# Optimization experiments

Hardware: AMD Instinct MI355X
Metric: run time of the kernel (lower is better)

## Reference

```python
import jax, jax.numpy as jnp
import numpy as np

EMBED_DIM = 1024
NUM_HEADS = 16
HEAD_DIM = EMBED_DIM // NUM_HEADS
FF_DIM = 4096
EPS = 1e-5


def layer_norm(x, gamma, beta):
    mu = jnp.mean(x, axis=-1, keepdims=True)
    var = jnp.var(x, axis=-1, keepdims=True)
    return (x - mu) * jax.lax.rsqrt(var + EPS) * gamma + beta


def setup_inputs() -> dict:
    key = jax.random.key(0)
    ks = jax.random.split(key, 10)
    B, S = 2, 2048
    sd = 1.0 / np.sqrt(EMBED_DIM)
    sf = 1.0 / np.sqrt(FF_DIM)
    return {
        "x": jax.random.normal(ks[0], (B, S, EMBED_DIM), jnp.float32),
        # grouped QKV: 3*num_heads groups, each embed_dim -> head_dim
        "Wqkv": jax.random.normal(ks[1], (3 * NUM_HEADS, EMBED_DIM, HEAD_DIM), jnp.float32) * sd,
        "bqkv": jnp.zeros((3 * NUM_HEADS, HEAD_DIM), jnp.float32),
        "Wo": jax.random.normal(ks[2], (EMBED_DIM, EMBED_DIM), jnp.float32) * sd,
        "bo": jnp.zeros((EMBED_DIM,), jnp.float32),
        "W1": jax.random.normal(ks[3], (EMBED_DIM, FF_DIM), jnp.float32) * sd,
        "b1": jnp.zeros((FF_DIM,), jnp.float32),
        "W2": jax.random.normal(ks[4], (FF_DIM, EMBED_DIM), jnp.float32) * sf,
        "b2": jnp.zeros((EMBED_DIM,), jnp.float32),
        "ln1_g": jnp.ones((EMBED_DIM,), jnp.float32),
        "ln1_b": jnp.zeros((EMBED_DIM,), jnp.float32),
        "ln2_g": jnp.ones((EMBED_DIM,), jnp.float32),
        "ln2_b": jnp.zeros((EMBED_DIM,), jnp.float32),
    }


def reference(x, Wqkv, bqkv, Wo, bo, W1, b1, W2, b2, ln1_g, ln1_b, ln2_g, ln2_b):
    B, S, D = x.shape
    normed = layer_norm(x, ln1_g, ln1_b)
    # grouped QKV projection: group g gets its own (D, head_dim) weight
    qkv = jnp.einsum('bsd,gdh->bgsh', normed, Wqkv) + bqkv[None, :, None, :]
    qkv = qkv.reshape(B, 3, NUM_HEADS, S, HEAD_DIM)
    q, k, v = qkv[:, 0], qkv[:, 1], qkv[:, 2]  # each [B, H, S, hd]
    attn = jnp.einsum('bhqd,bhkd->bhqk', q, k) / np.sqrt(HEAD_DIM)
    attn = jax.nn.softmax(attn, axis=-1)
    out = jnp.einsum('bhqk,bhkd->bhqd', attn, v)
    out = out.transpose(0, 2, 1, 3).reshape(B, S, D)
    out = out @ Wo + bo
    x = x + out
    normed2 = layer_norm(x, ln2_g, ln2_b)
    ff = jax.nn.relu(normed2 @ W1 + b1) @ W2 + b2
    return x + ff
```

## Files before the change

kernel.cpp:

```cpp
#include <hip/hip_runtime.h>
#include <stdint.h>

#define SEQ    2048
#define NB     2
#define NHEADS 16
#define HDIM   64
#define EMBED  1024
#define NROWS  (NB*SEQ)
#define QKVSZ  ((size_t)NB*NHEADS*SEQ*HDIM)

typedef __attribute__((ext_vector_type(8))) short short8;
typedef __attribute__((ext_vector_type(4))) float float4v;
typedef __attribute__((ext_vector_type(16))) float float16v;
typedef __attribute__((ext_vector_type(2))) unsigned int uint2v;
typedef __attribute__((ext_vector_type(4))) unsigned int uint4v;

__device__ __forceinline__ float b2f(unsigned short h) {
    unsigned int u = ((unsigned int)h) << 16;
    union { unsigned int u; float f; } c; c.u = u; return c.f;
}
__device__ __forceinline__ unsigned short f2b(float f) {
    union { float f; unsigned int u; } c; c.f = f;
    unsigned int u = c.u;
    u += 0x7FFFu + ((u >> 16) & 1u);
    return (unsigned short)(u >> 16);
}
__device__ __forceinline__ unsigned int fbits(float f) {
    union { float f; unsigned int u; } c; c.f = f; return c.u;
}
__device__ __forceinline__ unsigned int cvtpk_bf16(float lo, float hi) {
    unsigned int r;
    asm("v_cvt_pk_bf16_f32 %0, %1, %2" : "=v"(r) : "v"(lo), "v"(hi));
    return r;
}

__device__ __forceinline__ void gload_lds16(const void* g, void* l) {
    __builtin_amdgcn_global_load_lds(
        (const __attribute__((address_space(1))) unsigned int*)g,
        (__attribute__((address_space(3))) unsigned int*)l, 16, 0, 0);
}

__device__ __forceinline__ int probe_f32(const void* probe) {
    return ((const unsigned short*)probe)[0] == 0;
}
__device__ __forceinline__ float lde(const void* base, size_t off, int f32) {
    return f32 ? ((const float*)base)[off] : b2f(((const unsigned short*)base)[off]);
}
__device__ __forceinline__ void ste(void* base, size_t off, float v, int f32) {
    if (f32) ((float*)base)[off] = v;
    else     ((unsigned short*)base)[off] = f2b(v);
}

__global__ __launch_bounds__(256) void ln_kernel(
    const void* __restrict__ x,
    const void* __restrict__ g,
    const void* __restrict__ b,
    unsigned short* __restrict__ out,
    const void* __restrict__ probe)
{
    int f32 = probe_f32(probe);
    int row = blockIdx.x;
    int t = threadIdx.x;
    float v0, v1, v2, v3;
    if (f32) {
        float4 rv = ((const float4*)x)[(size_t)row * (EMBED / 4) + t];
        v0 = rv.x; v1 = rv.y; v2 = rv.z; v3 = rv.w;
    } else {
        ushort4 rv = ((const ushort4*)((const unsigned short*)x + (size_t)row * EMBED))[t];
        v0 = b2f(rv.x); v1 = b2f(rv.y); v2 = b2f(rv.z); v3 = b2f(rv.w);
    }
    float s  = v0 + v1 + v2 + v3;
    float sq = v0*v0 + v1*v1 + v2*v2 + v3*v3;
    #pragma unroll
    for (int off = 32; off > 0; off >>= 1) {
        s  += __shfl_xor(s,  off);
        sq += __shfl_xor(sq, off);
    }
    __shared__ float red[8];
    int lane = t & 63, wv = t >> 6;
    if (lane == 0) { red[wv] = s; red[wv + 4] = sq; }
    __syncthreads();
    s  = red[0] + red[1] + red[2] + red[3];
    sq = red[4] + red[5] + red[6] + red[7];
    float mu  = s * (1.0f / EMBED);
    float var = sq * (1.0f / EMBED) - mu * mu;
    float rs  = rsqrtf(var + 1e-5f);
    float g0 = lde(g, t*4+0, f32), g1 = lde(g, t*4+1, f32);
    float g2 = lde(g, t*4+2, f32), g3 = lde(g, t*4+3, f32);
    float b0 = lde(b, t*4+0, f32), b1 = lde(b, t*4+1, f32);
    float b2 = lde(b, t*4+2, f32), b3 = lde(b, t*4+3, f32);
    ushort4 ov;
    ov.x = f2b((v0 - mu) * rs * g0 + b0);
    ov.y = f2b((v1 - mu) * rs * g1 + b1);
    ov.z = f2b((v2 - mu) * rs * g2 + b2);
    ov.w = f2b((v3 - mu) * rs * g3 + b3);
    ((ushort4*)(out + (size_t)row * EMBED))[t] = ov;
}

template<int QKV>
__global__ __launch_bounds__(256) void transpose_kernel(
    const void* __restrict__ in,
    unsigned short* __restrict__ out, int K, int N,
    const void* __restrict__ probe)
{
    __shared__ unsigned short t[64 * 68];
    int f32 = probe_f32(probe);
    int tid = threadIdx.x;
    int n0 = blockIdx.x * 64, k0 = blockIdx.y * 64;
    #pragma unroll
    for (int i = 0; i < 4; i++) {
        int id = tid + i * 256;
        int kr = id >> 4, nc = (id & 15) * 4;
        size_t srcoff;
        if (QKV) srcoff = ((size_t)(n0 >> 6) << 16) + (size_t)(k0 + kr) * 64 + nc;
        else     srcoff = (size_t)(k0 + kr) * N + n0 + nc;
        ushort4 val;
        if (f32) {
            float4 rv = *(const float4*)((const float*)in + srcoff);
            val.x = f2b(rv.x); val.y = f2b(rv.y); val.z = f2b(rv.z); val.w = f2b(rv.w);
        } else {
            val = *(const ushort4*)((const unsigned short*)in + srcoff);
        }
        *(ushort4*)&t[kr * 68 + nc] = val;
    }
    __syncthreads();
    #pragma unroll
    for (int i = 0; i < 4; i++) {
        int id = tid + i * 256;
        int nr = id >> 4, kc = (id & 15) * 4;
        ushort4 o;
        o.x = t[(kc + 0) * 68 + nr];
        o.y = t[(kc + 1) * 68 + nr];
        o.z = t[(kc + 2) * 68 + nr];
        o.w = t[(kc + 3) * 68 + nr];
        *(ushort4*)(out + (size_t)(n0 + nr) * K + k0 + kc) = o;
    }
}

template<int DO_RELU, int HAS_BIAS, int OUTMODE>
__global__ __launch_bounds__(512) void gemm256_kernel(
    const unsigned short* __restrict__ A,
    const unsigned short* __restrict__ Bt,
    const void* __restrict__ bias,
    void* __restrict__ out,
    int M, int N, int Kloc, int ldA, int ldB,
    const void* __restrict__ probe)
{
    __shared__ unsigned short Als[2][256 * 64];
    __shared__ unsigned short Bls[2][256 * 64];
    int f32 = probe_f32(probe);
    int tid = threadIdx.x;
    int lane = tid & 63, wv = tid >> 6;
    int lq = lane >> 4, lr = lane & 15;
    int wr = wv >> 2, wc = wv & 3;
    int m0 = blockIdx.y * 256, n0 = blockIdx.x * 256;
    int k0 = blockIdx.z * Kloc;

    int srow = tid >> 3;
    int sch  = (tid & 7) ^ (srow & 7);
    const unsigned short* ga = A  + (size_t)(m0 + srow) * ldA + k0 + sch * 8;
    const unsigned short* gb = Bt + (size_t)(n0 + srow) * ldB + k0 + sch * 8;
    int ldst = tid * 8;
    int rx = lr & 7;

    float4v acc[8][4];
    #pragma unroll
    for (int i = 0; i < 8; i++)
        #pragma unroll
        for (int j = 0; j < 4; j++)
            { acc[i][j][0] = 0.f; acc[i][j][1] = 0.f; acc[i][j][2] = 0.f; acc[i][j][3] = 0.f; }

    int nkt = Kloc >> 6;
    #pragma unroll
    for (int u = 0; u < 4; u++)
        gload_lds16(ga + (size_t)u * 64 * ldA, &Als[0][u * 4096 + ldst]);
    #pragma unroll
    for (int u = 0; u < 4; u++)
        gload_lds16(gb + (size_t)u * 64 * ldB, &Bls[0][u * 4096 + ldst]);

    for (int kt = 0; kt < nkt; kt++) {
        int cur = kt & 1, nxt = cur ^ 1;
        if (kt + 1 < nkt) {
            int ko = (kt + 1) * 64;
            #pragma unroll
            for (int u = 0; u < 4; u++)
                gload_lds16(ga + (size_t)u * 64 * ldA + ko, &Als[nxt][u * 4096 + ldst]);
            asm volatile("s_waitcnt vmcnt(4)" ::: "memory");
        } else {
            asm volatile("s_waitcnt vmcnt(0)" ::: "memory");
        }
        __builtin_amdgcn_s_barrier();
        asm volatile("" ::: "memory");
        {
            short8 af[8], bf[4];
            #pragma unroll
            for (int mt = 0; mt < 8; mt++)
                af[mt] = *(const short8*)(
                    &Als[cur][(wr * 128 + mt * 16 + lr) * 64 + ((lq ^ rx) * 8)]);
            #pragma unroll
            for (int nt = 0; nt < 4; nt++)
                bf[nt] = *(const short8*)(
                    &Bls[cur][(wc * 64 + nt * 16 + lr) * 64 + ((lq ^ rx) * 8)]);
            __builtin_amdgcn_s_setprio(1);
            #pragma unroll
            for (int mt = 0; mt < 8; mt++)
                #pragma unroll
                for (int nt = 0; nt < 4; nt++)
                    acc[mt][nt] = __builtin_amdgcn_mfma_f32_16x16x32_bf16(af[mt], bf[nt], acc[mt][nt], 0, 0, 0);
            __builtin_amdgcn_s_setprio(0);
        }
        if (kt + 1 < nkt) {
            int ko = (kt + 1) * 64;
            #pragma unroll
            for (int u = 0; u < 4; u++)
                gload_lds16(gb + (size_t)u * 64 * ldB + ko, &Bls[nxt][u * 4096 + ldst]);
        }
        {
            short8 af[8], bf[4];
            #pragma unroll
            for (int mt = 0; mt < 8; mt++)
                af[mt] = *(const short8*)(
                    &Als[cur][(wr * 128 + mt * 16 + lr) * 64 + (((4 + lq) ^ rx) * 8)]);
            #pragma unroll
            for (int nt = 0; nt < 4; nt++)
                bf[nt] = *(const short8*)(
                    &Bls[cur][(wc * 64 + nt * 16 + lr) * 64 + (((4 + lq) ^ rx) * 8)]);
            __builtin_amdgcn_s_setprio(1);
            #pragma unroll
            for (int mt = 0; mt < 8; mt++)
                #pragma unroll
                for (int nt = 0; nt < 4; nt++)
                    acc[mt][nt] = __builtin_amdgcn_mfma_f32_16x16x32_bf16(af[mt], bf[nt], acc[mt][nt], 0, 0, 0);
            __builtin_amdgcn_s_setprio(0);
        }
        asm volatile("s_waitcnt lgkmcnt(0)" ::: "memory");
        __builtin_amdgcn_s_barrier();
    }

    if (OUTMODE == 3) {
        float* po = (float*)out + (size_t)blockIdx.z * M * N;
        #pragma unroll
        for (int mt = 0; mt < 8; mt++)
            #pragma unroll
            for (int nt = 0; nt < 4; nt++)
                #pragma unroll
                for (int rg = 0; rg < 4; rg++) {
                    int rr = m0 + wr * 128 + mt * 16 + lq * 4 + rg;
                    int cc = n0 + wc * 64 + nt * 16 + lr;
                    po[(size_t)rr * N + cc] = acc[mt][nt][rg];
                }
    } else if (OUTMODE == 2) {
        #pragma unroll
        for (int mt = 0; mt < 8; mt++) {
            int rrb = m0 + wr * 128 + mt * 16 + lq * 4;
            int bb = rrb >> 11, ss = rrb & 2047;
            #pragma unroll
            for (int nt = 0; nt < 4; nt++) {
                int cc = n0 + wc * 64 + nt * 16 + lr;
                int gg = cc >> 6, hd = cc & 63;
                int ty = gg >> 4, hh = gg & 15;
                float vv[4];
                #pragma unroll
                for (int rg = 0; rg < 4; rg++) {
                    float v = acc[mt][nt][rg];
                    if (HAS_BIAS) v += lde(bias, (size_t)cc, f32);
                    vv[rg] = v;
                }
                if (ty < 2) {
                    unsigned short* p = (unsigned short*)out + (size_t)ty * QKVSZ +
                        (((size_t)(bb * NHEADS + hh) * SEQ + ss) * HDIM) + hd;
                    #pragma unroll
                    for (int rg = 0; rg < 4; rg++) p[(size_t)rg * HDIM] = f2b(vv[rg]);
                } else {
                    ushort4 pk;
                    pk.x = f2b(vv[0]); pk.y = f2b(vv[1]);
                    pk.z = f2b(vv[2]); pk.w = f2b(vv[3]);
                    *(ushort4*)((unsigned short*)out + 2 * QKVSZ +
                        ((size_t)(bb * NHEADS + hh) * HDIM + hd) * SEQ + ss) = pk;
                }
            }
        }
    } else {
        #pragma unroll
        for (int mt = 0; mt < 8; mt++)
            #pragma unroll
            for (int nt = 0; nt < 4; nt++)
                #pragma unroll
                for (int rg = 0; rg < 4; rg++) {
                    int rr = m0 + wr * 128 + mt * 16 + lq * 4 + rg;
                    int cc = n0 + wc * 64 + nt * 16 + lr;
                    float v = acc[mt][nt][rg];
                    if (HAS_BIAS) v += lde(bias, (size_t)cc, f32);
                    if (DO_RELU) v = v > 0.f ? v : 0.f;
                    ((unsigned short*)out)[(size_t)rr * N + cc] = f2b(v);
                }
    }
}

template<int DO_RELU, int HAS_BIAS, int OUTMODE>
__global__ __launch_bounds__(512) void gemm256p8_kernel(
    const unsigned short* __restrict__ A,
    const unsigned short* __restrict__ Bt,
    const void* __restrict__ bias,
    void* __restrict__ out,
    int M, int N, int Kloc, int ldA, int ldB,
    const void* __restrict__ probe)
{
    __shared__ unsigned short Als[2][2][128 * 64];
    __shared__ unsigned short Bls[2][2][128 * 64];
    int f32 = probe_f32(probe);
    int tid = threadIdx.x;
    int lane = tid & 63, wv = tid >> 6;
    int lq = lane >> 4, lr = lane & 15;
    int wr = wv >> 2, wc = wv & 3;
    int m0 = blockIdx.y * 256, n0 = blockIdx.x * 256;
    int k0 = blockIdx.z * Kloc;

    int srow = tid >> 3;
    int sch  = (tid & 7) ^ (srow & 7);
    const unsigned short* ga = A  + (size_t)(m0 + srow) * ldA + k0 + sch * 8;
    const unsigned short* gb = Bt + (size_t)(n0 + srow) * ldB + k0 + sch * 8;
    int ldst = tid * 8;
    int rx = lr & 7;

    auto stA = [&](int d, int h, int ko) {
        gload_lds16(ga + (size_t)(h * 128) * ldA + ko, &Als[d][h][ldst]);
        gload_lds16(ga + (size_t)(h * 128 + 64) * ldA + ko, &Als[d][h][4096 + ldst]);
    };
    auto stB = [&](int d, int h, int ko) {
        gload_lds16(gb + (size_t)(h * 128) * ldB + ko, &Bls[d][h][ldst]);
        gload_lds16(gb + (size_t)(h * 128 + 64) * ldB + ko, &Bls[d][h][4096 + ldst]);
    };
    auto rdA = [&](int d, int qm, short8 (&af)[4][2]) {
        #pragma unroll
        for (int mt = 0; mt < 4; mt++)
            #pragma unroll
            for (int c = 0; c < 2; c++)
                af[mt][c] = *(const short8*)(&Als[d][qm][
                    (wr * 64 + mt * 16 + lr) * 64 + (((c * 4 + lq) ^ rx) * 8)]);
    };
    auto rdB = [&](int d, int qn, short8 (&bf)[2][2]) {
        #pragma unroll
        for (int nt = 0; nt < 2; nt++)
            #pragma unroll
            for (int c = 0; c < 2; c++)
                bf[nt][c] = *(const short8*)(&Bls[d][qn][
                    (wc * 32 + nt * 16 + lr) * 64 + (((c * 4 + lq) ^ rx) * 8)]);
    };
    auto MM = [&](short8 (&af)[4][2], short8 (&bf)[2][2], float4v (&aq)[4][2]) {
        __builtin_amdgcn_s_setprio(1);
        #pragma unroll
        for (int c = 0; c < 2; c++)
            #pragma unroll
            for (int mt = 0; mt < 4; mt++)
                #pragma unroll
                for (int nt = 0; nt < 2; nt++)
                    aq[mt][nt] = __builtin_amdgcn_mfma_f32_16x16x32_bf16(
                        af[mt][c], bf[nt][c], aq[mt][nt], 0, 0, 0);
        __builtin_amdgcn_s_setprio(0);
    };
    #define VMC(n)  asm volatile("s_waitcnt vmcnt(" #n ")" ::: "memory")
    #define BARF()  do { __builtin_amdgcn_s_barrier(); \
                         asm volatile("" ::: "memory"); } while (0)

    float4v acc00[4][2], acc01[4][2], acc11[4][2], acc10[4][2];
    #pragma unroll
    for (int i = 0; i < 4; i++)
        #pragma unroll
        for (int j = 0; j < 2; j++) {
            acc00[i][j] = float4v{0.f, 0.f, 0.f, 0.f};
            acc01[i][j] = float4v{0.f, 0.f, 0.f, 0.f};
            acc11[i][j] = float4v{0.f, 0.f, 0.f, 0.f};
            acc10[i][j] = float4v{0.f, 0.f, 0.f, 0.f};
        }
    short8 af0[4][2], af1[4][2], bf0[2][2], bf1[2][2];

    int nkt = Kloc >> 6;
    int npair = nkt >> 1;

    stA(0, 0, 0); stB(0, 0, 0); stB(0, 1, 0); stA(0, 1, 0);
    VMC(4); BARF();
    rdA(0, 0, af0); rdB(0, 0, bf0);

    for (int p = 0; p < npair - 1; p++) {
        int koB  = (2 * p + 1) * 64;
        int koA2 = (2 * p + 2) * 64;
        MM(af0, bf0, acc00); stA(1, 0, koB); VMC(4); BARF(); rdB(0, 1, bf1);
        MM(af0, bf1, acc01); stB(1, 0, koB); VMC(4); BARF(); rdA(0, 1, af1);
        MM(af1, bf1, acc11); stB(1, 1, koB);         BARF(); rdB(0, 0, bf0);
        MM(af1, bf0, acc10); stA(1, 1, koB); VMC(4); BARF(); rdA(1, 0, af0); rdB(1, 0, bf1);
        MM(af0, bf1, acc00); stA(0, 0, koA2); VMC(4); BARF(); rdB(1, 1, bf0);
        MM(af0, bf0, acc01); stB(0, 0, koA2); VMC(4); BARF(); rdA(1, 1, af1);
        MM(af1, bf0, acc11); stB(0, 1, koA2);         BARF(); rdB(1, 0, bf1);
        MM(af1, bf1, acc10); stA(0, 1, koA2); VMC(4); BARF(); rdA(0, 0, af0); rdB(0, 0, bf0);
    }
    {
        int koB = (nkt - 1) * 64;
        MM(af0, bf0, acc00); stA(1, 0, koB); VMC(4); BARF(); rdB(0, 1, bf1);
        MM(af0, bf1, acc01); stB(1, 0, koB); VMC(4); BARF(); rdA(0, 1, af1);
        MM(af1, bf1, acc11); stB(1, 1, koB);         BARF(); rdB(0, 0, bf0);
        MM(af1, bf0, acc10); stA(1, 1, koB); VMC(4); BARF(); rdA(1, 0, af0); rdB(1, 0, bf1);
        MM(af0, bf1, acc00);                  VMC(2); BARF(); rdB(1, 1, bf0);
        MM(af0, bf0, acc01);                  VMC(0); BARF(); rdA(1, 1, af1);
        MM(af1, bf0, acc11);                          BARF(); rdB(1, 0, bf1);
        MM(af1, bf1, acc10);
    }
    #undef VMC
    #undef BARF

    auto storeQ = [&](int qr, int qc, float4v (&aq)[4][2]) {
        if (OUTMODE == 3) {
            float* po = (float*)out + (size_t)blockIdx.z * M * N;
            #pragma unroll
            for (int mt = 0; mt < 4; mt++)
                #pragma unroll
                for (int nt = 0; nt < 2; nt++)
                    #pragma unroll
                    for (int rg = 0; rg < 4; rg++) {
                        int rr = m0 + qr * 128 + wr * 64 + mt * 16 + lq * 4 + rg;
                        int cc = n0 + qc * 128 + wc * 32 + nt * 16 + lr;
                        po[(size_t)rr * N + cc] = aq[mt][nt][rg];
                    }
        } else {
            #pragma unroll
            for (int mt = 0; mt < 4; mt++)
                #pragma unroll
                for (int nt = 0; nt < 2; nt++)
                    #pragma unroll
                    for (int rg = 0; rg < 4; rg++) {
                        int rr = m0 + qr * 128 + wr * 64 + mt * 16 + lq * 4 + rg;
                        int cc = n0 + qc * 128 + wc * 32 + nt * 16 + lr;
                        float v = aq[mt][nt][rg];
                        if (HAS_BIAS) v += lde(bias, (size_t)cc, f32);
                        if (DO_RELU) v = v > 0.f ? v : 0.f;
                        ((unsigned short*)out)[(size_t)rr * N + cc] = f2b(v);
                    }
        }
    };
    storeQ(0, 0, acc00); storeQ(0, 1, acc01);
    storeQ(1, 1, acc11); storeQ(1, 0, acc10);
}

__global__ __launch_bounds__(256) void ff2_combine_kernel(
    const float* __restrict__ part,
    const void* __restrict__ b2,
    void* __restrict__ xout,
    const void* __restrict__ probe)
{
    int f32 = probe_f32(probe);
    int row = blockIdx.x;
    int t = threadIdx.x;
    const size_t MN = (size_t)NROWS * EMBED;
    size_t base = (size_t)row * EMBED + t * 4;
    float4 p0 = *(const float4*)(part + base);
    float4 p1 = *(const float4*)(part + MN + base);
    float4 p2 = *(const float4*)(part + 2 * MN + base);
    float4 p3 = *(const float4*)(part + 3 * MN + base);
    float s0 = (p0.x + p1.x) + (p2.x + p3.x);
    float s1 = (p0.y + p1.y) + (p2.y + p3.y);
    float s2 = (p0.z + p1.z) + (p2.z + p3.z);
    float s3 = (p0.w + p1.w) + (p2.w + p3.w);
    int c = t * 4;
    s0 += lde(b2, c + 0, f32) + lde(xout, base + 0, f32);
    s1 += lde(b2, c + 1, f32) + lde(xout, base + 1, f32);
    s2 += lde(b2, c + 2, f32) + lde(xout, base + 2, f32);
    s3 += lde(b2, c + 3, f32) + lde(xout, base + 3, f32);
    ste(xout, base + 0, s0, f32);
    ste(xout, base + 1, s1, f32);
    ste(xout, base + 2, s2, f32);
    ste(xout, base + 3, s3, f32);
}

template<int DO_RELU, int HAS_BIAS, int HAS_RES, int OUTMODE>
__global__ __launch_bounds__(256) void gemm64_kernel(
    const unsigned short* __restrict__ A,
    const unsigned short* __restrict__ Bt,
    const void* __restrict__ bias,
    const void* __restrict__ res,
    void* __restrict__ out,
    int M, int N, int K, int ldA, int ldB,
    const void* __restrict__ probe)
{
    __shared__ unsigned short Als[2][64 * 32];
    __shared__ unsigned short Bls[2][64 * 32];
    int f32 = probe_f32(probe);
    int tid = threadIdx.x;
    int lane = tid & 63, wv = tid >> 6;
    int lq = lane >> 4, lr = lane & 15;
    int moff = (wv >> 1) * 32, noff = (wv & 1) * 32;
    int m0 = blockIdx.y * 64, n0 = blockIdx.x * 64;

    int rA = tid >> 2, jA = tid & 3;
    int jjA = jA ^ ((rA >> 1) & 3);
    const unsigned short* ga = A  + (size_t)(m0 + rA) * ldA + jjA * 8;
    const unsigned short* gb = Bt + (size_t)(n0 + rA) * ldB + jjA * 8;

    int fch = (lq ^ ((lr >> 1) & 3)) * 8;

    float4v acc[2][2];
    #pragma unroll
    for (int i = 0; i < 2; i++)
        #pragma unroll
        for (int j = 0; j < 2; j++)
            { acc[i][j][0] = 0.f; acc[i][j][1] = 0.f; acc[i][j][2] = 0.f; acc[i][j][3] = 0.f; }

    gload_lds16(ga, &Als[0][(size_t)tid * 8]);
    gload_lds16(gb, &Bls[0][(size_t)tid * 8]);

    int nkt = K >> 5;
    for (int kt = 0; kt < nkt; kt++) {
        int cur = kt & 1, nxt = cur ^ 1;
        __syncthreads();
        if (kt + 1 < nkt) {
            int ko = (kt + 1) * 32;
            gload_lds16(ga + ko, &Als[nxt][(size_t)tid * 8]);
            gload_lds16(gb + ko, &Bls[nxt][(size_t)tid * 8]);
        }
        short8 af[2], bfr[2];
        #pragma unroll
        for (int mt = 0; mt < 2; mt++)
            af[mt] = *(const short8*)(&Als[cur][(moff + mt * 16 + lr) * 32 + fch]);
        #pragma unroll
        for (int nt = 0; nt < 2; nt++)
            bfr[nt] = *(const short8*)(&Bls[cur][(noff + nt * 16 + lr) * 32 + fch]);
        #pragma unroll
        for (int mt = 0; mt < 2; mt++)
            #pragma unroll
            for (int nt = 0; nt < 2; nt++)
                acc[mt][nt] = __builtin_amdgcn_mfma_f32_16x16x32_bf16(af[mt], bfr[nt], acc[mt][nt], 0, 0, 0);
    }

    #pragma unroll
    for (int mt = 0; mt < 2; mt++) {
        #pragma unroll
        for (int nt = 0; nt < 2; nt++) {
            #pragma unroll
            for (int rg = 0; rg < 4; rg++) {
                int rr = m0 + moff + mt * 16 + lq * 4 + rg;
                int cc = n0 + noff + nt * 16 + lr;
                float v = acc[mt][nt][rg];
                if (HAS_BIAS) v += lde(bias, (size_t)cc, f32);
                if (DO_RELU) v = v > 0.f ? v : 0.f;
                if (HAS_RES) v += lde(res, (size_t)rr * N + cc, f32);
                if (OUTMODE == 1) ste(out, (size_t)rr * N + cc, v, f32);
                else ((unsigned short*)out)[(size_t)rr * N + cc] = f2b(v);
            }
        }
    }
}

__global__ __launch_bounds__(512) void attn_kernel(
    const unsigned short* __restrict__ qb,
    const unsigned short* __restrict__ kb,
    const unsigned short* __restrict__ vtb,
    unsigned short* __restrict__ outb)
{
    __shared__ unsigned short Kls[2][2][64 * 64];
    __shared__ unsigned short Vls[2][2][64 * 64];
    int tid = threadIdx.x;
    int lane = tid & 63, wv = tid >> 6;
    int l31 = lane & 31, hh = lane >> 5;
    int qg = wv & 3, half = wv >> 2;
    int bh = blockIdx.y;
    int b = bh >> 4, head = bh & 15;
    const unsigned short* q  = qb  + (size_t)bh * SEQ * HDIM;
    const unsigned short* k  = kb  + (size_t)bh * SEQ * HDIM;
    const unsigned short* vt = vtb + (size_t)bh * HDIM * SEQ;
    int q0w = blockIdx.x * 128 + qg * 32;

    const float C2 = 0.18033688011112042f;

    short8 qf[4];
    #pragma unroll
    for (int c = 0; c < 4; c++) {
        short8 raw = *(const short8*)(q + (size_t)(q0w + l31) * HDIM + c * 16 + hh * 8);
        #pragma unroll
        for (int j = 0; j < 8; j++)
            qf[c][j] = (short)f2b(b2f((unsigned short)raw[j]) * C2);
    }

    int ts = tid & 255;
    int rS = ts >> 3;
    int jjS = (ts & 7) ^ (rS & 7);
    const int NTH = SEQ / 128;
    int tbase = half * NTH;
    const unsigned short* gk0 = k + (size_t)rS * HDIM + jjS * 8;
    const unsigned short* gk1 = k + (size_t)(rS + 32) * HDIM + jjS * 8;
    const unsigned short* gv0 = vt + (size_t)rS * SEQ + jjS * 8;
    const unsigned short* gv1 = vt + (size_t)(rS + 32) * SEQ + jjS * 8;

    auto stage = [&](int bf, int tl) {
        int k0n = (tbase + tl) * 64;
        gload_lds16(gk0 + (size_t)k0n * HDIM, &Kls[half][bf][(size_t)ts * 8]);
        gload_lds16(gk1 + (size_t)k0n * HDIM, &Kls[half][bf][(size_t)(ts + 256) * 8]);
        gload_lds16(gv0 + k0n, &Vls[half][bf][(size_t)ts * 8]);
        gload_lds16(gv1 + k0n, &Vls[half][bf][(size_t)(ts + 256) * 8]);
    };

    float l_part = 0.f;
    float16v o0, o1;
    #pragma unroll
    for (int i = 0; i < 16; i++) { o0[i] = 0.f; o1[i] = 0.f; }

    stage(0, 0);

    for (int t = 0; t < NTH; t++) {
        int cur = t & 1;
        __builtin_amdgcn_s_barrier();
        asm volatile("" ::: "memory");
        if (t + 1 < NTH) {
            stage(cur ^ 1, t + 1);
            asm volatile("s_waitcnt vmcnt(4)" ::: "memory");
        } else {
            asm volatile("s_waitcnt vmcnt(0)" ::: "memory");
        }
        __builtin_amdgcn_s_barrier();
        asm volatile("" ::: "memory");

        float16v st0, st1;
        #pragma unroll
        for (int i = 0; i < 16; i++) { st0[i] = 0.f; st1[i] = 0.f; }
        {
            int r0 = l31, r1 = 32 + l31;
            int rxk = l31 & 7;
            __builtin_amdgcn_s_setprio(1);
            #pragma unroll
            for (int c = 0; c < 4; c++) {
                short8 kf0 = *(const short8*)(
                    &Kls[half][cur][r0 * 64 + (((2 * c + hh) ^ rxk) * 8)]);
                st0 = __builtin_amdgcn_mfma_f32_32x32x16_bf16(kf0, qf[c], st0, 0, 0, 0);
                short8 kf1 = *(const short8*)(
                    &Kls[half][cur][r1 * 64 + (((2 * c + hh) ^ rxk) * 8)]);
                st1 = __builtin_amdgcn_mfma_f32_32x32x16_bf16(kf1, qf[c], st1, 0, 0, 0);
            }
            __builtin_amdgcn_s_setprio(0);
        }

        int rv0 = l31, rv1 = 32 + l31;
        int rxv = l31 & 7;
        #pragma unroll
        for (int kb2 = 0; kb2 < 2; kb2++) {
            float p[16];
            #pragma unroll
            for (int rg = 0; rg < 16; rg++) {
                float sv = kb2 ? st1[rg] : st0[rg];
                p[rg] = __builtin_amdgcn_exp2f(sv);
                l_part += p[rg];
            }
            #pragma unroll
            for (int s = 0; s < 2; s++) {
                unsigned int a1 = cvtpk_bf16(p[8*s+0], p[8*s+1]);
                unsigned int a2 = cvtpk_bf16(p[8*s+2], p[8*s+3]);
                unsigned int b1 = cvtpk_bf16(p[8*s+4], p[8*s+5]);
                unsigned int b2 = cvtpk_bf16(p[8*s+6], p[8*s+7]);
                uint2v r1 = __builtin_amdgcn_permlane32_swap(a1, b1, false, false);
                uint2v r2 = __builtin_amdgcn_permlane32_swap(a2, b2, false, false);
                union { uint4v u; short8 s8; } pun;
                pun.u.x = r1.x; pun.u.y = r2.x; pun.u.z = r1.y; pun.u.w = r2.y;
                short8 pf = pun.s8;
                int g = kb2 * 2 + s;
                short8 vf0 = *(const short8*)(
                    &Vls[half][cur][rv0 * 64 + (((2 * g + hh) ^ rxv) * 8)]);
                short8 vf1 = *(const short8*)(
                    &Vls[half][cur][rv1 * 64 + (((2 * g + hh) ^ rxv) * 8)]);
                __builtin_amdgcn_s_setprio(1);
                o0 = __builtin_amdgcn_mfma_f32_32x32x16_bf16(pf, vf0, o0, 0, 0, 0);
                o1 = __builtin_amdgcn_mfma_f32_32x32x16_bf16(pf, vf1, o1, 0, 0, 0);
                __builtin_amdgcn_s_setprio(0);
            }
        }
    }

    l_part += __shfl_xor(l_part, 32);

    __syncthreads();
    float* obuf = (float*)&Kls[0][0][0];
    float* lbuf = (float*)&Vls[0][0][0];
    if (half == 1) {
        float* od = obuf + (size_t)qg * 2048 + lane * 4;
        #pragma unroll
        for (int ib = 0; ib < 4; ib++) {
            float4 v4;
            v4.x = o0[ib*4+0]; v4.y = o0[ib*4+1]; v4.z = o0[ib*4+2]; v4.w = o0[ib*4+3];
            *(float4*)(od + ib * 256) = v4;
        }
        #pragma unroll
        for (int ib = 0; ib < 4; ib++) {
            float4 v4;
            v4.x = o1[ib*4+0]; v4.y = o1[ib*4+1]; v4.z = o1[ib*4+2]; v4.w = o1[ib*4+3];
            *(float4*)(od + (ib + 4) * 256) = v4;
        }
        if (hh == 0) lbuf[qg * 32 + l31] = l_part;
    }
    __syncthreads();
    if (half == 0) {
        float* od = obuf + (size_t)qg * 2048 + lane * 4;
        #pragma unroll
        for (int ib = 0; ib < 4; ib++) {
            float4 v4 = *(const float4*)(od + ib * 256);
            o0[ib*4+0] += v4.x; o0[ib*4+1] += v4.y; o0[ib*4+2] += v4.z; o0[ib*4+3] += v4.w;
        }
        #pragma unroll
        for (int ib = 0; ib < 4; ib++) {
            float4 v4 = *(const float4*)(od + (ib + 4) * 256);
            o1[ib*4+0] += v4.x; o1[ib*4+1] += v4.y; o1[ib*4+2] += v4.z; o1[ib*4+3] += v4.w;
        }
        float linv_me = 1.f / (l_part + lbuf[qg * 32 + l31]);
        #pragma unroll
        for (int rg = 0; rg < 16; rg++) {
            int qrow = (rg & 3) + 8 * (rg >> 2) + 4 * hh;
            float linv = __shfl(linv_me, qrow);
            size_t rowbase = ((size_t)(b * SEQ + q0w + qrow)) * EMBED + head * HDIM;
            outb[rowbase + l31]      = f2b(o0[rg] * linv);
            outb[rowbase + 32 + l31] = f2b(o1[rg] * linv);
        }
    }
}

extern "C" void kernel_launch(void* const* d_in, const int* in_sizes, int n_in,
                              void* d_out, int out_size, void* d_ws, size_t ws_size,
                              hipStream_t stream)
{
    (void)in_sizes; (void)n_in; (void)out_size;
    const void* x    = d_in[0];
    const void* Wqkv = d_in[1];
    const void* bqkv = d_in[2];
    const void* Wo   = d_in[3];
    const void* bo   = d_in[4];
    const void* W1   = d_in[5];
    const void* b1   = d_in[6];
    const void* W2   = d_in[7];
    const void* b2   = d_in[8];
    const void* g1   = d_in[9];
    const void* be1  = d_in[10];
    const void* g2   = d_in[11];
    const void* be2  = d_in[12];
    const void* probe = g1;

    char* ws = (char*)d_ws;
    const size_t MB = 1024 * 1024;
    unsigned short* tmp1  = (unsigned short*)(ws + 0 * MB);
    unsigned short* qkv   = (unsigned short*)(ws + 8 * MB);
    unsigned short* WoT   = (unsigned short*)(ws + 8 * MB);
    unsigned short* W1T   = (unsigned short*)(ws + 8 * MB);
    unsigned short* W2T   = (unsigned short*)(ws + 8 * MB);
    unsigned short* h1    = (unsigned short*)(ws + 16 * MB);
    float*          part  = (float*)(ws + 48 * MB);
    unsigned short* WqkvT = (unsigned short*)d_out;
    bool splitk_ok = ws_size >= (size_t)112 * MB;

    transpose_kernel<1><<<dim3(3072 / 64, 1024 / 64), 256, 0, stream>>>(Wqkv, WqkvT, 1024, 3072, probe);
    ln_kernel<<<dim3(NROWS), 256, 0, stream>>>(x, g1, be1, tmp1, probe);
    gemm256_kernel<0, 1, 2><<<dim3(3072 / 256, NROWS / 256), 512, 0, stream>>>(
        tmp1, WqkvT, bqkv, qkv, NROWS, 3072, 1024, 1024, 1024, probe);
    attn_kernel<<<dim3(SEQ / 128, NB * NHEADS), 512, 0, stream>>>(
        qkv, qkv + QKVSZ, qkv + 2 * QKVSZ, tmp1);
    transpose_kernel<0><<<dim3(1024 / 64, 1024 / 64), 256, 0, stream>>>(Wo, WoT, 1024, 1024, probe);
    gemm64_kernel<0, 1, 1, 1><<<dim3(1024 / 64, NROWS / 64), 256, 0, stream>>>(
        tmp1, WoT, bo, x, d_out, NROWS, 1024, 1024, 1024, 1024, probe);
    ln_kernel<<<dim3(NROWS), 256, 0, stream>>>(d_out, g2, be2, tmp1, probe);
    transpose_kernel<0><<<dim3(4096 / 64, 1024 / 64), 256, 0, stream>>>(W1, W1T, 1024, 4096, probe);
    gemm256p8_kernel<1, 1, 0><<<dim3(4096 / 256, NROWS / 256), 512, 0, stream>>>(
        tmp1, W1T, b1, h1, NROWS, 4096, 1024, 1024, 1024, probe);
    transpose_kernel<0><<<dim3(1024 / 64, 4096 / 64), 256, 0, stream>>>(W2, W2T, 4096, 1024, probe);
    if (splitk_ok) {
        gemm256p8_kernel<0, 0, 3><<<dim3(1024 / 256, NROWS / 256, 4), 512, 0, stream>>>(
            h1, W2T, nullptr, part, NROWS, 1024, 1024, 4096, 4096, probe);
        ff2_combine_kernel<<<dim3(NROWS), 256, 0, stream>>>(part, b2, d_out, probe);
    } else {
        gemm64_kernel<0, 1, 1, 1><<<dim3(1024 / 64, NROWS / 64), 256, 0, stream>>>(
            h1, W2T, b2, d_out, d_out, NROWS, 1024, 4096, 4096, 4096, probe);
    }
}
```

Baseline: 370.0 us.

## Use gemm256p8 for QKV projection and add XCD-aware block swizzling

Removes the older gemm256 kernel and routes the QKV projection through gemm256p8, which gains an OUTMODE 2 epilogue that scatters into the per-head Q/K/V layout with V transposed. Adds an XCD swizzle that remaps linear block ids so consecutive tiles land on the same XCD, applied to gemm256p8 and to the attention kernel. The intent is better L2 reuse of shared A/B tiles and K/V heads within each chiplet, and using the presumably faster p8 GEMM schedule for QKV. The swizzle only applies when the block count is a multiple of 8. Otherwise the mapping is unchanged.

```diff
diff --git a/kernel.cpp b/kernel.cpp
--- a/kernel.cpp
+++ b/kernel.cpp
@@ -49,6 +49,11 @@
 __device__ __forceinline__ void ste(void* base, size_t off, float v, int f32) {
     if (f32) ((float*)base)[off] = v;
     else     ((unsigned short*)base)[off] = f2b(v);
+}
+
+__device__ __forceinline__ int xcd_swz(int bid, int nb) {
+    if (nb & 7) return bid;
+    return (bid & 7) * (nb >> 3) + (bid >> 3);
 }
 
 __global__ __launch_bounds__(256) void ln_kernel(
@@ -138,166 +143,6 @@
 }
 
 template<int DO_RELU, int HAS_BIAS, int OUTMODE>
-__global__ __launch_bounds__(512) void gemm256_kernel(
-    const unsigned short* __restrict__ A,
-    const unsigned short* __restrict__ Bt,
-    const void* __restrict__ bias,
-    void* __restrict__ out,
-    int M, int N, int Kloc, int ldA, int ldB,
-    const void* __restrict__ probe)
-{
-    __shared__ unsigned short Als[2][256 * 64];
-    __shared__ unsigned short Bls[2][256 * 64];
-    int f32 = probe_f32(probe);
-    int tid = threadIdx.x;
-    int lane = tid & 63, wv = tid >> 6;
-    int lq = lane >> 4, lr = lane & 15;
-    int wr = wv >> 2, wc = wv & 3;
-    int m0 = blockIdx.y * 256, n0 = blockIdx.x * 256;
-    int k0 = blockIdx.z * Kloc;
-
-    int srow = tid >> 3;
-    int sch  = (tid & 7) ^ (srow & 7);
-    const unsigned short* ga = A  + (size_t)(m0 + srow) * ldA + k0 + sch * 8;
-    const unsigned short* gb = Bt + (size_t)(n0 + srow) * ldB + k0 + sch * 8;
-    int ldst = tid * 8;
-    int rx = lr & 7;
-
-    float4v acc[8][4];
-    #pragma unroll
-    for (int i = 0; i < 8; i++)
-        #pragma unroll
-        for (int j = 0; j < 4; j++)
-            { acc[i][j][0] = 0.f; acc[i][j][1] = 0.f; acc[i][j][2] = 0.f; acc[i][j][3] = 0.f; }
-
-    int nkt = Kloc >> 6;
-    #pragma unroll
-    for (int u = 0; u < 4; u++)
-        gload_lds16(ga + (size_t)u * 64 * ldA, &Als[0][u * 4096 + ldst]);
-    #pragma unroll
-    for (int u = 0; u < 4; u++)
-        gload_lds16(gb + (size_t)u * 64 * ldB, &Bls[0][u * 4096 + ldst]);
-
-    for (int kt = 0; kt < nkt; kt++) {
-        int cur = kt & 1, nxt = cur ^ 1;
-        if (kt + 1 < nkt) {
-            int ko = (kt + 1) * 64;
-            #pragma unroll
-            for (int u = 0; u < 4; u++)
-                gload_lds16(ga + (size_t)u * 64 * ldA + ko, &Als[nxt][u * 4096 + ldst]);
-            asm volatile("s_waitcnt vmcnt(4)" ::: "memory");
-        } else {
-            asm volatile("s_waitcnt vmcnt(0)" ::: "memory");
-        }
-        __builtin_amdgcn_s_barrier();
-        asm volatile("" ::: "memory");
-        {
-            short8 af[8], bf[4];
-            #pragma unroll
-            for (int mt = 0; mt < 8; mt++)
-                af[mt] = *(const short8*)(
-                    &Als[cur][(wr * 128 + mt * 16 + lr) * 64 + ((lq ^ rx) * 8)]);
-            #pragma unroll
-            for (int nt = 0; nt < 4; nt++)
-                bf[nt] = *(const short8*)(
-                    &Bls[cur][(wc * 64 + nt * 16 + lr) * 64 + ((lq ^ rx) * 8)]);
-            __builtin_amdgcn_s_setprio(1);
-            #pragma unroll
-            for (int mt = 0; mt < 8; mt++)
-                #pragma unroll
-                for (int nt = 0; nt < 4; nt++)
-                    acc[mt][nt] = __builtin_amdgcn_mfma_f32_16x16x32_bf16(af[mt], bf[nt], acc[mt][nt], 0, 0, 0);
-            __builtin_amdgcn_s_setprio(0);
-        }
-        if (kt + 1 < nkt) {
-            int ko = (kt + 1) * 64;
-            #pragma unroll
-            for (int u = 0; u < 4; u++)
-                gload_lds16(gb + (size_t)u * 64 * ldB + ko, &Bls[nxt][u * 4096 + ldst]);
-        }
-        {
-            short8 af[8], bf[4];
-            #pragma unroll
-            for (int mt = 0; mt < 8; mt++)
-                af[mt] = *(const short8*)(
-                    &Als[cur][(wr * 128 + mt * 16 + lr) * 64 + (((4 + lq) ^ rx) * 8)]);
-            #pragma unroll
-            for (int nt = 0; nt < 4; nt++)
-                bf[nt] = *(const short8*)(
-                    &Bls[cur][(wc * 64 + nt * 16 + lr) * 64 + (((4 + lq) ^ rx) * 8)]);
-            __builtin_amdgcn_s_setprio(1);
-            #pragma unroll
-            for (int mt = 0; mt < 8; mt++)
-                #pragma unroll
-                for (int nt = 0; nt < 4; nt++)
-                    acc[mt][nt] = __builtin_amdgcn_mfma_f32_16x16x32_bf16(af[mt], bf[nt], acc[mt][nt], 0, 0, 0);
-            __builtin_amdgcn_s_setprio(0);
-        }
-        asm volatile("s_waitcnt lgkmcnt(0)" ::: "memory");
-        __builtin_amdgcn_s_barrier();
-    }
-
-    if (OUTMODE == 3) {
-        float* po = (float*)out + (size_t)blockIdx.z * M * N;
-        #pragma unroll
-        for (int mt = 0; mt < 8; mt++)
-            #pragma unroll
-            for (int nt = 0; nt < 4; nt++)
-                #pragma unroll
-                for (int rg = 0; rg < 4; rg++) {
-                    int rr = m0 + wr * 128 + mt * 16 + lq * 4 + rg;
-                    int cc = n0 + wc * 64 + nt * 16 + lr;
-                    po[(size_t)rr * N + cc] = acc[mt][nt][rg];
-                }
-    } else if (OUTMODE == 2) {
-        #pragma unroll
-        for (int mt = 0; mt < 8; mt++) {
-            int rrb = m0 + wr * 128 + mt * 16 + lq * 4;
-            int bb = rrb >> 11, ss = rrb & 2047;
-            #pragma unroll
-            for (int nt = 0; nt < 4; nt++) {
-                int cc = n0 + wc * 64 + nt * 16 + lr;
-                int gg = cc >> 6, hd = cc & 63;
-                int ty = gg >> 4, hh = gg & 15;
-                float vv[4];
-                #pragma unroll
-                for (int rg = 0; rg < 4; rg++) {
-                    float v = acc[mt][nt][rg];
-                    if (HAS_BIAS) v += lde(bias, (size_t)cc, f32);
-                    vv[rg] = v;
-                }
-                if (ty < 2) {
-                    unsigned short* p = (unsigned short*)out + (size_t)ty * QKVSZ +
-                        (((size_t)(bb * NHEADS + hh) * SEQ + ss) * HDIM) + hd;
-                    #pragma unroll
-                    for (int rg = 0; rg < 4; rg++) p[(size_t)rg * HDIM] = f2b(vv[rg]);
-                } else {
-                    ushort4 pk;
-                    pk.x = f2b(vv[0]); pk.y = f2b(vv[1]);
-                    pk.z = f2b(vv[2]); pk.w = f2b(vv[3]);
-                    *(ushort4*)((unsigned short*)out + 2 * QKVSZ +
-                        ((size_t)(bb * NHEADS + hh) * HDIM + hd) * SEQ + ss) = pk;
-                }
-            }
-        }
-    } else {
-        #pragma unroll
-        for (int mt = 0; mt < 8; mt++)
-            #pragma unroll
-            for (int nt = 0; nt < 4; nt++)
-                #pragma unroll
-                for (int rg = 0; rg < 4; rg++) {
-                    int rr = m0 + wr * 128 + mt * 16 + lq * 4 + rg;
-                    int cc = n0 + wc * 64 + nt * 16 + lr;
-                    float v = acc[mt][nt][rg];
-                    if (HAS_BIAS) v += lde(bias, (size_t)cc, f32);
-                    if (DO_RELU) v = v > 0.f ? v : 0.f;
-                    ((unsigned short*)out)[(size_t)rr * N + cc] = f2b(v);
-                }
-    }
-}
-
-template<int DO_RELU, int HAS_BIAS, int OUTMODE>
 __global__ __launch_bounds__(512) void gemm256p8_kernel(
     const unsigned short* __restrict__ A,
     const unsigned short* __restrict__ Bt,
@@ -313,7 +158,9 @@
     int lane = tid & 63, wv = tid >> 6;
     int lq = lane >> 4, lr = lane & 15;
     int wr = wv >> 2, wc = wv & 3;
-    int m0 = blockIdx.y * 256, n0 = blockIdx.x * 256;
+    int gx = gridDim.x;
+    int bid = xcd_swz(blockIdx.y * gx + blockIdx.x, gx * gridDim.y);
+    int m0 = (bid / gx) * 256, n0 = (bid % gx) * 256;
     int k0 = blockIdx.z * Kloc;
 
     int srow = tid >> 3;
@@ -421,6 +268,37 @@
                         int cc = n0 + qc * 128 + wc * 32 + nt * 16 + lr;
                         po[(size_t)rr * N + cc] = aq[mt][nt][rg];
                     }
+        } else if (OUTMODE == 2) {
+            #pragma unroll
+            for (int mt = 0; mt < 4; mt++) {
+                int rrb = m0 + qr * 128 + wr * 64 + mt * 16 + lq * 4;
+                int bb = rrb >> 11, ss = rrb & 2047;
+                #pragma unroll
+                for (int nt = 0; nt < 2; nt++) {
+                    int cc = n0 + qc * 128 + wc * 32 + nt * 16 + lr;
+                    int gg = cc >> 6, hd = cc & 63;
+                    int ty = gg >> 4, hq = gg & 15;
+                    float vv[4];
+                    #pragma unroll
+                    for (int rg = 0; rg < 4; rg++) {
+                        float v = aq[mt][nt][rg];
+                        if (HAS_BIAS) v += lde(bias, (size_t)cc, f32);
+                        vv[rg] = v;
+                    }
+                    if (ty < 2) {
+                        unsigned short* p = (unsigned short*)out + (size_t)ty * QKVSZ +
+                            (((size_t)(bb * NHEADS + hq) * SEQ + ss) * HDIM) + hd;
+                        #pragma unroll
+                        for (int rg = 0; rg < 4; rg++) p[(size_t)rg * HDIM] = f2b(vv[rg]);
+                    } else {
+                        ushort4 pk;
+                        pk.x = f2b(vv[0]); pk.y = f2b(vv[1]);
+                        pk.z = f2b(vv[2]); pk.w = f2b(vv[3]);
+                        *(ushort4*)((unsigned short*)out + 2 * QKVSZ +
+                            ((size_t)(bb * NHEADS + hq) * HDIM + hd) * SEQ + ss) = pk;
+                    }
+                }
+            }
         } else {
             #pragma unroll
             for (int mt = 0; mt < 4; mt++)
@@ -561,12 +439,14 @@
     int lane = tid & 63, wv = tid >> 6;
     int l31 = lane & 31, hh = lane >> 5;
     int qg = wv & 3, half = wv >> 2;
-    int bh = blockIdx.y;
+    int gx = gridDim.x;
+    int bid = xcd_swz(blockIdx.y * gx + blockIdx.x, gx * gridDim.y);
+    int bx = bid % gx, bh = bid / gx;
     int b = bh >> 4, head = bh & 15;
     const unsigned short* q  = qb  + (size_t)bh * SEQ * HDIM;
     const unsigned short* k  = kb  + (size_t)bh * SEQ * HDIM;
     const unsigned short* vt = vtb + (size_t)bh * HDIM * SEQ;
-    int q0w = blockIdx.x * 128 + qg * 32;
+    int q0w = bx * 128 + qg * 32;
 
     const float C2 = 0.18033688011112042f;
 
@@ -751,7 +631,7 @@
 
     transpose_kernel<1><<<dim3(3072 / 64, 1024 / 64), 256, 0, stream>>>(Wqkv, WqkvT, 1024, 3072, probe);
     ln_kernel<<<dim3(NROWS), 256, 0, stream>>>(x, g1, be1, tmp1, probe);
-    gemm256_kernel<0, 1, 2><<<dim3(3072 / 256, NROWS / 256), 512, 0, stream>>>(
+    gemm256p8_kernel<0, 1, 2><<<dim3(3072 / 256, NROWS / 256), 512, 0, stream>>>(
         tmp1, WqkvT, bqkv, qkv, NROWS, 3072, 1024, 1024, 1024, probe);
     attn_kernel<<<dim3(SEQ / 128, NB * NHEADS), 512, 0, stream>>>(
         qkv, qkv + QKVSZ, qkv + 2 * QKVSZ, tmp1);
```

After: 377.4 us. 2.0% more time.
